# Kernel tuning notes

Measured on AMD Instinct MI355X. Metric: run time of the kernel, lower is better.

Reference implementation:

```python
import jax, jax.numpy as jnp
import numpy as np
import math

B, L, M, D, EL, H = 128, 105, 55, 256, 3, 1
PATCH = [3, 5, 7]

def pos_embed(T, d):
    pos = jnp.arange(T, dtype=jnp.float32)[:, None]
    div = jnp.exp(jnp.arange(0, d, 2, dtype=jnp.float32) * (-math.log(10000.0) / d))
    pe = jnp.zeros((T, d), dtype=jnp.float32)
    pe = pe.at[:, 0::2].set(jnp.sin(pos * div))
    pe = pe.at[:, 1::2].set(jnp.cos(pos * div))
    return pe

def circular_conv(x, w):
    # x: [N, T, Cin], w: [Dout, Cin, 3]; Conv1d kernel 3, circular padding 1, no bias
    xc = jnp.pad(x.transpose(0, 2, 1), ((0, 0), (0, 0), (1, 1)), mode='wrap')
    y = jax.lax.conv_general_dilated(xc, w, (1,), 'VALID', dimension_numbers=('NCH', 'OIH', 'NCH'))
    return y.transpose(0, 2, 1)

def _forward(x, conv_p0, conv_n0, conv_p1, conv_n1, conv_p2, conv_n2, Wq, bq, Wk, bk):
    convs = [(conv_p0, conv_n0), (conv_p1, conv_n1), (conv_p2, conv_n2)]
    # RevIN 'norm': per-sample standardization over time; stats are detached in torch
    mean = jax.lax.stop_gradient(jnp.mean(x, axis=1, keepdims=True))
    std = jax.lax.stop_gradient(jnp.sqrt(jnp.var(x, axis=1, keepdims=True) + 1e-5))
    xr = (x - mean) / std                      # [B, L, M]
    xt = xr.transpose(0, 2, 1)                 # [B, M, L]
    dk = D // H
    scale = 1.0 / math.sqrt(dk)
    series_list, prior_list = [], []
    for i, p in enumerate(PATCH):
        n = L // p
        # patch-size branch: (b m) n p -> embed over n with in_channels=p
        x_size = circular_conv(xt.reshape(B * M, n, p), convs[i][0]) + pos_embed(n, D)
        # patch-num branch: (b m) p n -> embed over p with in_channels=n
        x_num = circular_conv(xt.reshape(B * M, p, n), convs[i][1]) + pos_embed(p, D)
        for l in range(EL):
            def attn_mean(z):
                T = z.shape[1]
                q = (z @ Wq[l] + bq[l]).reshape(B * M, T, H, dk)
                k = (z @ Wk[l] + bk[l]).reshape(B * M, T, H, dk)
                a = jax.nn.softmax(scale * jnp.einsum('blhe,bshe->bhls', q, k), axis=-1)
                # fuse: mean over channel BEFORE expanding to window size
                # (repeat/tile commutes with the channel-mean, avoids [B*M,H,L,L])
                return a.reshape(B, M, H, T, T).mean(axis=1)   # [B, H, T, T]
            a_size = attn_mean(x_size)                          # [B, H, n, n]
            # einops repeat '(m rm) (n rn)': element-wise contiguous repeat
            series_list.append(jnp.repeat(jnp.repeat(a_size, p, axis=-2), p, axis=-1))
            a_num = attn_mean(x_num)                            # [B, H, p, p]
            # torch .repeat: tiling
            prior_list.append(jnp.tile(a_num, (1, 1, n, n)))
    # order: patch-major, layer-minor (matches the flattened lists)
    return jnp.stack(series_list), jnp.stack(prior_list)        # each [9, B, H, L, L]

def setup_inputs():
    key = jax.random.key(0)
    ks = jax.random.split(key, 12)
    s = 0.05
    inp = {"x": jax.random.normal(ks[0], (B, L, M), jnp.float32)}
    for i, p in enumerate(PATCH):
        inp[f"conv_p{i}"] = s * jax.random.normal(ks[1 + 2 * i], (D, p, 3), jnp.float32)
        inp[f"conv_n{i}"] = s * jax.random.normal(ks[2 + 2 * i], (D, L // p, 3), jnp.float32)
    inp["Wq"] = s * jax.random.normal(ks[7], (EL, D, D), jnp.float32)
    inp["bq"] = jnp.zeros((EL, D), jnp.float32)
    inp["Wk"] = s * jax.random.normal(ks[8], (EL, D, D), jnp.float32)
    inp["bk"] = jnp.zeros((EL, D), jnp.float32)
    return inp

def reference(x, conv_p0, conv_n0, conv_p1, conv_n1, conv_p2, conv_n2, Wq, bq, Wk, bk):
    return _forward(x, conv_p0, conv_n0, conv_p1, conv_n1, conv_p2, conv_n2, Wq, bq, Wk, bk)
```

## Files before the change

kernel.cpp:

```cpp
#include <hip/hip_runtime.h>
#include <hip/hip_bf16.h>

#define B_ 128
#define L_ 105
#define M_ 55
#define D_ 256
#define NCOMBO 18

#define WS_XT    0
#define WS_PE    739200
#define WS_LEFT  761216
#define WS_RIGHT 1258880
#define WS_MM    1756544
#define WS_MP    761216
#define WS_ACC   1258880
#define LR_STRIDE 27648
#define MM_STRIDE 11664
#define MP_STRIDE 12544
#define ACC_TOT  758016

#define WS_LRP        1966592
#define LRP_KZ_STRIDE 27648
#define LRP_C_STRIDE  110592
#define LRP_HALF      1990656
#define WS_NEED_BYTES ((size_t)(WS_LRP + 2 * LRP_HALF) * 4)

__constant__ int c_peOff[6] = {0, 35, 38, 59, 64, 79};
__constant__ int c_accbase[18] = {0,1225,2450, 3675,3684,3693, 3702,4143,4584,
                                  5025,5050,5075, 5100,5325,5550, 5775,5824,5873};

__device__ __forceinline__ void combo_dims(int c, int& i, int& br, int& l,
                                           int& p, int& n, int& Cin, int& T, int& J) {
    i = c / 6; br = (c % 6) / 3; l = c % 3;
    p = 3 + 2 * i;
    n = L_ / p;
    Cin = br ? n : p;
    T   = br ? p : n;
    J = 3 * Cin;
}

#define PREP_REVIN_BLOCKS 3520
#define PREP_BLOCKS (PREP_REVIN_BLOCKS + 6)
__global__ __launch_bounds__(256) void prep_kernel(const float* __restrict__ x,
                                                   float* __restrict__ ws) {
    int bid = blockIdx.x;
    if (bid < PREP_REVIN_BLOCKS) {
        int tid2 = threadIdx.x & 127;
        int half = threadIdx.x >> 7;
        int bm = bid * 2 + half;
        int b = bm / M_, m = bm % M_;
        __shared__ float s1[2][128], s2[2][128];
        float v = 0.f;
        if (tid2 < L_) v = x[(b * L_ + tid2) * M_ + m];
        s1[half][tid2] = v; s2[half][tid2] = v * v;
        __syncthreads();
        for (int off = 64; off > 0; off >>= 1) {
            if (tid2 < off) {
                s1[half][tid2] += s1[half][tid2 + off];
                s2[half][tid2] += s2[half][tid2 + off];
            }
            __syncthreads();
        }
        float mean = s1[half][0] * (1.f / L_);
        float var  = s2[half][0] * (1.f / L_) - mean * mean;
        float rstd = rsqrtf(var + 1e-5f);
        if (tid2 < L_) ws[WS_XT + bm * L_ + tid2] = (v - mean) * rstd;
    } else {
        int bi = bid - PREP_REVIN_BLOCKS;
        int i = bi / 2, br = bi % 2;
        int p = 3 + 2 * i, n = L_ / p;
        int T = br ? p : n;
        int d = threadIdx.x;
        float divv = expf(-(float)(d & ~1) * (logf(10000.f) / (float)D_));
        float* base = ws + WS_PE + c_peOff[bi] * D_;
        for (int t = 0; t < T; ++t) {
            float arg = (float)t * divv;
            base[t * D_ + d] = (d & 1) ? cosf(arg) : sinf(arg);
        }
    }
}

__global__ __launch_bounds__(256) void lr2_kernel(
                          const float* __restrict__ w0, const float* __restrict__ w1,
                          const float* __restrict__ w2c, const float* __restrict__ w3,
                          const float* __restrict__ w4, const float* __restrict__ w5,
                          const float* __restrict__ Wq, const float* __restrict__ bq,
                          const float* __restrict__ Wk, const float* __restrict__ bk,
                          float* __restrict__ ws) {
    int c = blockIdx.x;
    int i, br, l, p, n, Cin, T, J; combo_dims(c, i, br, l, p, n, Cin, T, J);
    int Mdim = J + T;
    int r0 = blockIdx.y * 8;
    if (r0 >= Mdim) return;
    int kz = blockIdx.z;
    int d0 = kz * 64;
    int wi = i * 2 + br;
    const float* conv = (wi == 0) ? w0 : (wi == 1) ? w1 : (wi == 2) ? w2c
                       : (wi == 3) ? w3 : (wi == 4) ? w4 : w5;
    __shared__ float S[8][64];
    int tid = threadIdx.x;
    for (int idx = tid; idx < 8 * 64; idx += 256) {
        int rr = idx >> 6, dd = idx & 63;
        int row = r0 + rr; float val = 0.f;
        int d = d0 + dd;
        if (row < J) val = conv[d * J + row];
        else if (row < Mdim) val = ws[WS_PE + (c_peOff[wi] + (row - J)) * D_ + d];
        S[rr][dd] = val;
    }
    __syncthreads();
    const float* wqp = Wq + l * D_ * D_;
    const float* wkp = Wk + l * D_ * D_;
    float accL[8], accR[8];
#pragma unroll
    for (int rr = 0; rr < 8; ++rr) { accL[rr] = 0.f; accR[rr] = 0.f; }
    int o = tid;
#pragma unroll 8
    for (int dd = 0; dd < 64; ++dd) {
        int d = d0 + dd;
        float wqv = wqp[d * D_ + o];
        float wkv = wkp[d * D_ + o];
#pragma unroll
        for (int rr = 0; rr < 8; ++rr) {
            float sv = S[rr][dd];
            accL[rr] += sv * wqv;
            accR[rr] += sv * wkv;
        }
    }
    float bqv = (kz == 0) ? bq[l * D_ + o] : 0.f;
    float bkv = (kz == 0) ? bk[l * D_ + o] : 0.f;
    float* Lp = ws + WS_LRP + c * LRP_C_STRIDE + kz * LRP_KZ_STRIDE;
    float* Rp = Lp + LRP_HALF;
#pragma unroll
    for (int rr = 0; rr < 8; ++rr) {
        int row = r0 + rr;
        if (row < Mdim) {
            float aq = (row >= J) ? bqv : 0.f;
            float ak = (row >= J) ? bkv : 0.f;
            Lp[row * D_ + o] = accL[rr] + aq;
            Rp[row * D_ + o] = accR[rr] + ak;
        }
    }
}

__global__ __launch_bounds__(256) void lr_kernel(
                          const float* __restrict__ w0, const float* __restrict__ w1,
                          const float* __restrict__ w2c, const float* __restrict__ w3,
                          const float* __restrict__ w4, const float* __restrict__ w5,
                          const float* __restrict__ Wq, const float* __restrict__ bq,
                          const float* __restrict__ Wk, const float* __restrict__ bk,
                          float* __restrict__ ws) {
    int c = blockIdx.x;
    int i, br, l, p, n, Cin, T, J; combo_dims(c, i, br, l, p, n, Cin, T, J);
    int Mdim = J + T;
    int r0 = blockIdx.y * 4;
    if (r0 >= Mdim) return;
    int wi = i * 2 + br;
    const float* conv = (wi == 0) ? w0 : (wi == 1) ? w1 : (wi == 2) ? w2c
                       : (wi == 3) ? w3 : (wi == 4) ? w4 : w5;
    __shared__ float S[4][256];
    int tid = threadIdx.x;
    for (int idx = tid; idx < 4 * 256; idx += 256) {
        int rr = idx >> 8, dd = idx & 255;
        int row = r0 + rr; float val = 0.f;
        if (row < J) val = conv[dd * J + row];
        else if (row < Mdim) val = ws[WS_PE + (c_peOff[wi] + (row - J)) * D_ + dd];
        S[rr][dd] = val;
    }
    __syncthreads();
    const float* wqp = Wq + l * D_ * D_;
    const float* wkp = Wk + l * D_ * D_;
    float accL[4], accR[4];
#pragma unroll
    for (int rr = 0; rr < 4; ++rr) { accL[rr] = 0.f; accR[rr] = 0.f; }
    int o = tid;
#pragma unroll 8
    for (int d = 0; d < D_; ++d) {
        float wqv = wqp[d * D_ + o];
        float wkv = wkp[d * D_ + o];
#pragma unroll
        for (int rr = 0; rr < 4; ++rr) {
            float sv = S[rr][d];
            accL[rr] += sv * wqv;
            accR[rr] += sv * wkv;
        }
    }
    float bqv = bq[l * D_ + o], bkv = bk[l * D_ + o];
#pragma unroll
    for (int rr = 0; rr < 4; ++rr) {
        int row = r0 + rr;
        if (row < Mdim) {
            float aq = (row >= J) ? bqv : 0.f;
            float ak = (row >= J) ? bkv : 0.f;
            ws[WS_LEFT  + c * LR_STRIDE + row * D_ + o] = accL[rr] + aq;
            ws[WS_RIGHT + c * LR_STRIDE + row * D_ + o] = accR[rr] + ak;
        }
    }
}

__global__ void mm_kernel(float* __restrict__ ws, int use_partial) {
    int c = blockIdx.x;
    int i, br, l, p, n, Cin, T, J; combo_dims(c, i, br, l, p, n, Cin, T, J);
    int Mdim = J + T;
    int tr = blockIdx.y / 7, tc = blockIdx.y % 7;
    int r0 = tr * 16, c0 = tc * 16;
    if (r0 >= Mdim || c0 >= Mdim) return;
    __shared__ __align__(16) float Lb[16][260], Rb[16][260];
    int tid = threadIdx.x;
    if (use_partial) {
        const float* Lp = ws + WS_LRP + c * LRP_C_STRIDE;
        const float* Rp = Lp + LRP_HALF;
        for (int idx = tid; idx < 16 * 256; idx += 256) {
            int rr = idx >> 8, d = idx & 255;
            int rL = r0 + rr, rR = c0 + rr;
            float lv = 0.f, rv = 0.f;
            if (rL < Mdim) {
                int base = rL * D_ + d;
                lv = Lp[base] + Lp[base + LRP_KZ_STRIDE]
                   + Lp[base + 2 * LRP_KZ_STRIDE] + Lp[base + 3 * LRP_KZ_STRIDE];
            }
            if (rR < Mdim) {
                int base = rR * D_ + d;
                rv = Rp[base] + Rp[base + LRP_KZ_STRIDE]
                   + Rp[base + 2 * LRP_KZ_STRIDE] + Rp[base + 3 * LRP_KZ_STRIDE];
            }
            Lb[rr][d] = lv; Rb[rr][d] = rv;
        }
    } else {
        for (int idx = tid; idx < 16 * 256; idx += 256) {
            int rr = idx >> 8, d = idx & 255;
            int rL = r0 + rr, rR = c0 + rr;
            Lb[rr][d] = (rL < Mdim) ? ws[WS_LEFT  + c * LR_STRIDE + rL * D_ + d] : 0.f;
            Rb[rr][d] = (rR < Mdim) ? ws[WS_RIGHT + c * LR_STRIDE + rR * D_ + d] : 0.f;
        }
    }
    __syncthreads();
    int rr = tid / 16, cc = tid % 16;
    const float4* lrow = (const float4*)(&Lb[rr][0]);
    const float4* rrow = (const float4*)(&Rb[cc][0]);
    float acc = 0.f;
#pragma unroll 8
    for (int d4 = 0; d4 < 64; ++d4) {
        float4 a = lrow[d4], bb = rrow[d4];
        acc += a.x * bb.x + a.y * bb.y + a.z * bb.z + a.w * bb.w;
    }
    int r = r0 + rr, cth = c0 + cc;
    if (r < Mdim && cth < Mdim)
        ws[WS_MM + c * MM_STRIDE + r * Mdim + cth] = acc;
}

__global__ void pack_kernel(float* __restrict__ ws) {
    int c = blockIdx.x;
    int i, br, l, p, n, Cin, T, J; combo_dims(c, i, br, l, p, n, Cin, T, J);
    int Mdim = J + T;
    int Cinp = (Cin + 3) & ~3;
    int Jp = 3 * Cinp;
    int T4 = (T + 3) & ~3;
    int W = Jp + T4;
    const float* MMc = ws + WS_MM + c * MM_STRIDE;
    float* Mp = ws + WS_MP + c * MP_STRIDE;
    for (int e = blockIdx.y * 256 + threadIdx.x; e < W * W; e += 16 * 256) {
        int r = e / W, o = e % W;
        int srcr = -1, srcc = -1;
        bool brow = false;
        if (r < Jp) {
            int k = r / Cinp, cin = r % Cinp;
            if (cin < Cin) srcr = cin * 3 + k;
        } else {
            int t = r - Jp;
            if (t < T) { srcr = J + t; brow = true; }
        }
        if (o < Jp) {
            int k2 = o / Cinp, cin2 = o % Cinp;
            if (cin2 < Cin) srcc = cin2 * 3 + k2;
        } else {
            int s = o - Jp;
            if (s < T) srcc = J + s;
        }
        float val;
        if (srcr >= 0 && srcc >= 0) val = MMc[srcr * Mdim + srcc];
        else if (brow && o >= Jp && srcc < 0) val = -1e30f;
        else val = 0.f;
        Mp[e] = val;
    }
}

__global__ void zero_acc(float* __restrict__ ws) {
    int idx = blockIdx.x * 256 + threadIdx.x;
    if (idx < ACC_TOT / 4) {
        float4 z; z.x = 0.f; z.y = 0.f; z.z = 0.f; z.w = 0.f;
        ((float4*)(ws + WS_ACC))[idx] = z;
    }
}

template<int P, int BR>
__global__ __launch_bounds__(256) void attn2(const float* __restrict__ ws,
                                             float* __restrict__ wsw) {
    constexpr int N    = L_ / P;
    constexpr int Cin  = BR ? N : P;
    constexpr int T    = BR ? P : N;
    constexpr int Cinp = (Cin + 3) & ~3;
    constexpr int Jp   = 3 * Cinp;
    constexpr int JP4  = Jp / 4;
    constexpr int T4   = (T + 3) & ~3;
    constexpr int W    = Jp + T4;
    constexpr int W4   = W / 4;
    constexpr int ST   = T4 + 1;
    constexpr int II   = (P - 3) / 2;
    constexpr int MC   = BR ? (P == 3 ? 12 : 8) : (P == 7 ? 8 : 4);
    constexpr int TH   = (BR == 0 && P == 3) ? 2 : 1;
    constexpr int TSUB = (T + TH - 1) / TH;
    constexpr int GR   = MC * TSUB + 1;
    constexpr int NT   = (MC / 4) * TSUB * W4;
    constexpr int TPB  = (NT + 255) / 256;
    constexpr int MCQ  = MC / 4;
    constexpr int CQ   = Cinp / 4;
    constexpr int CQP  = CQ | 1;
    constexpr int S4N  = T4 / 4;
    constexpr int XTR4 = Cinp * MCQ + 1;

    constexpr int OFF_X2A = 0;
    constexpr int SZ_X2A  = MC * T * CQP * 4;
    constexpr int OFF_G   = OFF_X2A + SZ_X2A;
    constexpr int SZ_G    = 4 * W4 * GR;
    constexpr int OFF_X2T = OFF_G + SZ_G;
    constexpr int SZ_X2T  = T * XTR4 * 4;
    constexpr int OFF_MSL = OFF_X2T + SZ_X2T;
    constexpr int SZ_MSL  = BR ? 0 : Cinp * W;
    constexpr int OFF_S   = OFF_X2T;
    constexpr int SZ_S    = MC * TSUB * ST;
    constexpr int END_A   = OFF_MSL + SZ_MSL;
    constexpr int END_B   = OFF_S + SZ_S;
    constexpr int TOT     = (END_A > END_B) ? END_A : END_B;
    static_assert(TOT * 4 <= 65536, "LDS budget");

    __shared__ __align__(16) float smem[TOT];
    const int tid = threadIdx.x;
    const int b = blockIdx.x, l = blockIdx.y;
    const int sp = blockIdx.z / TH;
    const int th = blockIdx.z % TH;
    const int t0 = th * TSUB;
    const int TC = (T - t0 < TSUB) ? (T - t0) : TSUB;
    const int c = II * 6 + BR * 3 + l;
    const int m0 = sp * MC;
    const int vm = (M_ - m0 < MC) ? (M_ - m0) : MC;

    const float*  Mpg  = ws + WS_MP + c * MP_STRIDE;
    const float4* Mpg4 = (const float4*)Mpg;

    for (int e = tid; e < MC * T * CQP * 4; e += 256) {
        int cin  = e % (CQP * 4);
        int trow = (e / (CQP * 4)) % T;
        int mcol = e / (CQP * 4 * T);
        float v = 0.f;
        if (cin < Cin && m0 + mcol < M_)
            v = ws[WS_XT + (size_t)(b * M_ + m0 + mcol) * L_ + trow * Cin + cin];
        smem[OFF_X2A + e] = v;
    }
    for (int e = tid; e < T * XTR4 * 4; e += 256) {
        int w    = e % (XTR4 * 4);
        int trow = e / (XTR4 * 4);
        float v = 0.f;
        if (w < Cinp * MC) {
            int mcol = w % MC, cin = w / MC;
            if (cin < Cin && m0 + mcol < M_)
                v = ws[WS_XT + (size_t)(b * M_ + m0 + mcol) * L_ + trow * Cin + cin];
        }
        smem[OFF_X2T + e] = v;
    }
    __syncthreads();

    const float4* X2T4 = (const float4*)(smem + OFF_X2T);
    const float4* X2A4 = (const float4*)(smem + OFF_X2A);
    float4*       MSL4 = (float4*)(smem + OFF_MSL);
    float4*       G4w  = (float4*)(smem + OFF_G);
    const float4* G4   = (const float4*)(smem + OFF_G);

    float a[TPB][4][4];
#pragma unroll
    for (int tt = 0; tt < TPB; ++tt) {
        int q = tid + tt * 256;
        if (q < NT) {
            int o4 = q % W4, tl = (q / W4) % TSUB;
            if (tl < TC) {
                float4 bv = Mpg4[(Jp + t0 + tl) * W4 + o4];
#pragma unroll
                for (int am = 0; am < 4; ++am) {
                    a[tt][am][0] = bv.x; a[tt][am][1] = bv.y;
                    a[tt][am][2] = bv.z; a[tt][am][3] = bv.w;
                }
            }
        }
    }
    if constexpr (BR == 0) {
        for (int k = 0; k < 3; ++k) {
            for (int e = tid; e < Cinp * W4; e += 256)
                MSL4[e] = Mpg4[k * Cinp * W4 + e];
            __syncthreads();
#pragma unroll
            for (int tt = 0; tt < TPB; ++tt) {
                int q = tid + tt * 256;
                if (q < NT) {
                    int o4 = q % W4, tl = (q / W4) % TSUB, m4 = q / (W4 * TSUB);
                    if (tl < TC) {
                        int trow = t0 + tl + k - 1;
                        if (trow < 0) trow += T;
                        if (trow >= T) trow -= T;
                        const float4* xp = X2T4 + trow * XTR4 + m4;
                        const float4* mp = MSL4 + o4;
#pragma unroll 4
                        for (int cin = 0; cin < Cinp; ++cin) {
                            float4 x4 = xp[cin * MCQ];
                            float4 mv = mp[cin * W4];
#pragma unroll
                            for (int aq = 0; aq < 4; ++aq) {
                                float m = (aq == 0) ? mv.x : (aq == 1) ? mv.y
                                        : (aq == 2) ? mv.z : mv.w;
                                a[tt][0][aq] += x4.x * m;
                                a[tt][1][aq] += x4.y * m;
                                a[tt][2][aq] += x4.z * m;
                                a[tt][3][aq] += x4.w * m;
                            }
                        }
                    }
                }
            }
            __syncthreads();
        }
    } else {
        __syncthreads();
#pragma unroll
        for (int k = 0; k < 3; ++k) {
#pragma unroll
            for (int tt = 0; tt < TPB; ++tt) {
                int q = tid + tt * 256;
                if (q < NT) {
                    int o4 = q % W4, tl = (q / W4) % TSUB, m4 = q / (W4 * TSUB);
                    if (tl < TC) {
                        int trow = t0 + tl + k - 1;
                        if (trow < 0) trow += T;
                        if (trow >= T) trow -= T;
                        const float4* xp = X2T4 + trow * XTR4 + m4;
                        const float4* mp = Mpg4 + k * Cinp * W4 + o4;
#pragma unroll 4
                        for (int cin = 0; cin < Cinp; ++cin) {
                            float4 x4 = xp[cin * MCQ];
                            float4 mv = mp[cin * W4];
#pragma unroll
                            for (int aq = 0; aq < 4; ++aq) {
                                float m = (aq == 0) ? mv.x : (aq == 1) ? mv.y
                                        : (aq == 2) ? mv.z : mv.w;
                                a[tt][0][aq] += x4.x * m;
                                a[tt][1][aq] += x4.y * m;
                                a[tt][2][aq] += x4.z * m;
                                a[tt][3][aq] += x4.w * m;
                            }
                        }
                    }
                }
            }
        }
    }
#pragma unroll
    for (int tt = 0; tt < TPB; ++tt) {
        int q = tid + tt * 256;
        if (q < NT) {
            int o4 = q % W4, tl = (q / W4) % TSUB, m4 = q / (W4 * TSUB);
            if (tl < TC) {
#pragma unroll
                for (int am = 0; am < 4; ++am) {
                    float4 o;
                    o.x = a[tt][am][0]; o.y = a[tt][am][1];
                    o.z = a[tt][am][2]; o.w = a[tt][am][3];
                    G4w[o4 * GR + (m4 * 4 + am) * TSUB + tl] = o;
                }
            }
        }
    }
    __syncthreads();

    for (int it = tid; it < MC * TSUB * S4N; it += 256) {
        int tl = it % TSUB;
        int s4 = (it / TSUB) % S4N;
        int mc = it / (TSUB * S4N);
        if (tl >= TC) continue;
        int mrow = mc * TSUB + tl;
        float4 bi = G4[(JP4 + s4) * GR + mrow];
        float acc[4] = {bi.x, bi.y, bi.z, bi.w};
#pragma unroll 2
        for (int cinq = 0; cinq < CQ; ++cinq) {
            float4 xr[6];
#pragma unroll
            for (int kk = 0; kk < 6; ++kk) {
                int r = s4 * 4 - 1 + kk;
                if (r < 0) r += T;
                if (r >= T) r -= T;
                xr[kk] = X2A4[(mc * T + r) * CQP + cinq];
            }
#pragma unroll
            for (int k = 0; k < 3; ++k) {
                float4 g = G4[(k * CQ + cinq) * GR + mrow];
#pragma unroll
                for (int q = 0; q < 4; ++q) {
                    float4 x4 = xr[q + k];
                    acc[q] += g.x * x4.x + g.y * x4.y + g.z * x4.z + g.w * x4.w;
                }
            }
        }
#pragma unroll
        for (int q = 0; q < 4; ++q)
            smem[OFF_S + (mc * TSUB + tl) * ST + s4 * 4 + q] = 0.0625f * acc[q];
    }
    __syncthreads();

    for (int rid = tid; rid < MC * TSUB; rid += 256) {
        int mc = rid / TSUB, tl = rid % TSUB;
        if (tl >= TC) continue;
        int base = OFF_S + (mc * TSUB + tl) * ST;
        float pr[T4];
#pragma unroll
        for (int s = 0; s < T4; ++s) pr[s] = smem[base + s];
        float mx = -1e30f;
#pragma unroll
        for (int s = 0; s < T4; ++s) mx = fmaxf(mx, pr[s]);
        float sum = 0.f;
#pragma unroll
        for (int s = 0; s < T4; ++s) { pr[s] = __expf(pr[s] - mx); sum += pr[s]; }
        float inv = 1.f / sum;
#pragma unroll
        for (int s = 0; s < T; ++s) smem[base + s] = pr[s] * inv;
    }
    __syncthreads();

    float* accp = wsw + WS_ACC + c_accbase[c] * 128 + b * T * T;
    for (int e = tid; e < TC * T; e += 256) {
        int tl = e / T, s = e % T;
        float v = 0.f;
        for (int mc = 0; mc < vm; ++mc)
            v += smem[OFF_S + (mc * TSUB + tl) * ST + s];
        atomicAdd(&accp[(t0 + tl) * T + s], v);
    }
}

template<int P, int BR>
__device__ __forceinline__ void expand_body(const float* __restrict__ acc,
                                            float* __restrict__ outp) {
    constexpr int T = BR ? P : (L_ / P);
    for (int idx = threadIdx.x; idx < L_ * L_; idx += 256) {
        int r = idx / L_, c2 = idx % L_;
        int rt = BR ? (r % P) : (r / P);
        int ct = BR ? (c2 % P) : (c2 / P);
        outp[idx] = acc[rt * T + ct];
    }
}

__global__ __launch_bounds__(256) void expand_kernel(const float* __restrict__ ws,
                                                     float* __restrict__ out) {
    int c = blockIdx.x, b = blockIdx.y;
    int i = c / 6, br = (c % 6) / 3, l = c % 3;
    int p = 3 + 2 * i;
    int T = br ? p : (L_ / p);
    __shared__ float sAcc[1232];
    int abase = c_accbase[c] * 128 + b * T * T;
    for (int idx = threadIdx.x; idx < T * T; idx += 256)
        sAcc[idx] = ws[WS_ACC + abase + idx] * (1.f / (float)M_);
    __syncthreads();
    float* outp = out + ((size_t)(br * 9 + i * 3 + l) * B_ + (size_t)b) * (size_t)(L_ * L_);
    int key = i * 2 + br;
    switch (key) {
        case 0: expand_body<3, 0>(sAcc, outp); break;
        case 1: expand_body<3, 1>(sAcc, outp); break;
        case 2: expand_body<5, 0>(sAcc, outp); break;
        case 3: expand_body<5, 1>(sAcc, outp); break;
        case 4: expand_body<7, 0>(sAcc, outp); break;
        case 5: expand_body<7, 1>(sAcc, outp); break;
    }
}

extern "C" void kernel_launch(void* const* d_in, const int* in_sizes, int n_in,
                              void* d_out, int out_size, void* d_ws, size_t ws_size,
                              hipStream_t stream) {
    const float* x   = (const float*)d_in[0];
    const float* cp0 = (const float*)d_in[1];
    const float* cn0 = (const float*)d_in[2];
    const float* cp1 = (const float*)d_in[3];
    const float* cn1 = (const float*)d_in[4];
    const float* cp2 = (const float*)d_in[5];
    const float* cn2 = (const float*)d_in[6];
    const float* Wq  = (const float*)d_in[7];
    const float* bq  = (const float*)d_in[8];
    const float* Wk  = (const float*)d_in[9];
    const float* bk  = (const float*)d_in[10];
    float* ws = (float*)d_ws;
    float* out = (float*)d_out;

    const int use_partial = (ws_size >= WS_NEED_BYTES) ? 1 : 0;

    hipLaunchKernelGGL(prep_kernel, dim3(PREP_BLOCKS), dim3(256), 0, stream, x, ws);
    if (use_partial) {
        hipLaunchKernelGGL(lr2_kernel, dim3(NCOMBO, 14, 4), dim3(256), 0, stream,
                           cp0, cn0, cp1, cn1, cp2, cn2, Wq, bq, Wk, bk, ws);
    } else {
        hipLaunchKernelGGL(lr_kernel, dim3(NCOMBO, 27), dim3(256), 0, stream,
                           cp0, cn0, cp1, cn1, cp2, cn2, Wq, bq, Wk, bk, ws);
    }
    hipLaunchKernelGGL(mm_kernel, dim3(NCOMBO, 49), dim3(256), 0, stream, ws, use_partial);
    hipLaunchKernelGGL(pack_kernel, dim3(NCOMBO, 16), dim3(256), 0, stream, ws);
    hipLaunchKernelGGL(zero_acc, dim3((ACC_TOT / 4 + 255) / 256), dim3(256), 0, stream, ws);

    hipLaunchKernelGGL((attn2<3, 0>), dim3(B_, 3, 28), dim3(256), 0, stream, ws, ws);
    hipLaunchKernelGGL((attn2<3, 1>), dim3(B_, 3, 5),  dim3(256), 0, stream, ws, ws);
    hipLaunchKernelGGL((attn2<5, 0>), dim3(B_, 3, 14), dim3(256), 0, stream, ws, ws);
    hipLaunchKernelGGL((attn2<5, 1>), dim3(B_, 3, 7),  dim3(256), 0, stream, ws, ws);
    hipLaunchKernelGGL((attn2<7, 0>), dim3(B_, 3, 7),  dim3(256), 0, stream, ws, ws);
    hipLaunchKernelGGL((attn2<7, 1>), dim3(B_, 3, 7),  dim3(256), 0, stream, ws, ws);

    hipLaunchKernelGGL(expand_kernel, dim3(NCOMBO, B_), dim3(256), 0, stream, ws, out);
}
```

Baseline: 444.5 us.

## Fuse pack into mm_kernel writes and load full Mp slice into LDS once

The mm_kernel now writes its results directly in the packed, padded Mp layout, and the padding entries are initialised in prep_kernel. This removes the separate pack_kernel launch when the partial workspace path is active. The BR==0 attention kernel now loads all three k-slices of Mp into LDS once instead of reloading per k with barriers in between. The cost is more LDS per block, which may reduce occupancy.

```diff
diff --git a/kernel.cpp b/kernel.cpp
--- a/kernel.cpp
+++ b/kernel.cpp
@@ -40,7 +40,7 @@
 }
 
 #define PREP_REVIN_BLOCKS 3520
-#define PREP_BLOCKS (PREP_REVIN_BLOCKS + 6)
+#define PREP_BLOCKS (PREP_REVIN_BLOCKS + 6 + NCOMBO)
 __global__ __launch_bounds__(256) void prep_kernel(const float* __restrict__ x,
                                                    float* __restrict__ ws) {
     int bid = blockIdx.x;
@@ -65,7 +65,7 @@
         float var  = s2[half][0] * (1.f / L_) - mean * mean;
         float rstd = rsqrtf(var + 1e-5f);
         if (tid2 < L_) ws[WS_XT + bm * L_ + tid2] = (v - mean) * rstd;
-    } else {
+    } else if (bid < PREP_REVIN_BLOCKS + 6) {
         int bi = bid - PREP_REVIN_BLOCKS;
         int i = bi / 2, br = bi % 2;
         int p = 3 + 2 * i, n = L_ / p;
@@ -76,6 +76,22 @@
         for (int t = 0; t < T; ++t) {
             float arg = (float)t * divv;
             base[t * D_ + d] = (d & 1) ? cosf(arg) : sinf(arg);
+        }
+    } else {
+        int c = bid - (PREP_REVIN_BLOCKS + 6);
+        int i, br, l, p, n, Cin, T, J; combo_dims(c, i, br, l, p, n, Cin, T, J);
+        int Cinp = (Cin + 3) & ~3;
+        int Jp = 3 * Cinp;
+        int T4 = (T + 3) & ~3;
+        int W = Jp + T4;
+        float* Mp = ws + WS_MP + c * MP_STRIDE;
+        for (int e = threadIdx.x; e < W * W; e += 256) {
+            int r = e / W, o = e % W;
+            bool vr   = (r < Jp) ? ((r % Cinp) < Cin) : (r - Jp < T);
+            bool brow = (r >= Jp) && (r - Jp < T);
+            bool vc   = (o < Jp) ? ((o % Cinp) < Cin) : (o - Jp < T);
+            if (!(vr && vc))
+                Mp[e] = (brow && o >= Jp && !vc) ? -1e30f : 0.f;
         }
     }
 }
@@ -244,8 +260,18 @@
         acc += a.x * bb.x + a.y * bb.y + a.z * bb.z + a.w * bb.w;
     }
     int r = r0 + rr, cth = c0 + cc;
-    if (r < Mdim && cth < Mdim)
-        ws[WS_MM + c * MM_STRIDE + r * Mdim + cth] = acc;
+    if (r < Mdim && cth < Mdim) {
+        if (use_partial) {
+            int Cinp = (Cin + 3) & ~3;
+            int Jp = 3 * Cinp;
+            int W = Jp + ((T + 3) & ~3);
+            int rp = (r   < J) ? ((r   % 3) * Cinp + r   / 3) : (Jp + r   - J);
+            int op = (cth < J) ? ((cth % 3) * Cinp + cth / 3) : (Jp + cth - J);
+            ws[WS_MP + c * MP_STRIDE + rp * W + op] = acc;
+        } else {
+            ws[WS_MM + c * MM_STRIDE + r * Mdim + cth] = acc;
+        }
+    }
 }
 
 __global__ void pack_kernel(float* __restrict__ ws) {
@@ -325,7 +351,7 @@
     constexpr int OFF_X2T = OFF_G + SZ_G;
     constexpr int SZ_X2T  = T * XTR4 * 4;
     constexpr int OFF_MSL = OFF_X2T + SZ_X2T;
-    constexpr int SZ_MSL  = BR ? 0 : Cinp * W;
+    constexpr int SZ_MSL  = BR ? 0 : Jp * W;
     constexpr int OFF_S   = OFF_X2T;
     constexpr int SZ_S    = MC * TSUB * ST;
     constexpr int END_A   = OFF_MSL + SZ_MSL;
@@ -367,11 +393,15 @@
         }
         smem[OFF_X2T + e] = v;
     }
+    float4* MSL4 = (float4*)(smem + OFF_MSL);
+    if constexpr (BR == 0) {
+        for (int e = tid; e < Jp * W4; e += 256)
+            MSL4[e] = ((const float4*)Mpg)[e];
+    }
     __syncthreads();
 
     const float4* X2T4 = (const float4*)(smem + OFF_X2T);
     const float4* X2A4 = (const float4*)(smem + OFF_X2A);
-    float4*       MSL4 = (float4*)(smem + OFF_MSL);
     float4*       G4w  = (float4*)(smem + OFF_G);
     const float4* G4   = (const float4*)(smem + OFF_G);
 
@@ -391,69 +421,34 @@
             }
         }
     }
-    if constexpr (BR == 0) {
-        for (int k = 0; k < 3; ++k) {
-            for (int e = tid; e < Cinp * W4; e += 256)
-                MSL4[e] = Mpg4[k * Cinp * W4 + e];
-            __syncthreads();
-#pragma unroll
-            for (int tt = 0; tt < TPB; ++tt) {
-                int q = tid + tt * 256;
-                if (q < NT) {
-                    int o4 = q % W4, tl = (q / W4) % TSUB, m4 = q / (W4 * TSUB);
-                    if (tl < TC) {
-                        int trow = t0 + tl + k - 1;
-                        if (trow < 0) trow += T;
-                        if (trow >= T) trow -= T;
-                        const float4* xp = X2T4 + trow * XTR4 + m4;
-                        const float4* mp = MSL4 + o4;
+#pragma unroll
+    for (int k = 0; k < 3; ++k) {
+#pragma unroll
+        for (int tt = 0; tt < TPB; ++tt) {
+            int q = tid + tt * 256;
+            if (q < NT) {
+                int o4 = q % W4, tl = (q / W4) % TSUB, m4 = q / (W4 * TSUB);
+                if (tl < TC) {
+                    int trow = t0 + tl + k - 1;
+                    if (trow < 0) trow += T;
+                    if (trow >= T) trow -= T;
+                    const float4* xp = X2T4 + trow * XTR4 + m4;
 #pragma unroll 4
-                        for (int cin = 0; cin < Cinp; ++cin) {
-                            float4 x4 = xp[cin * MCQ];
-                            float4 mv = mp[cin * W4];
-#pragma unroll
-                            for (int aq = 0; aq < 4; ++aq) {
-                                float m = (aq == 0) ? mv.x : (aq == 1) ? mv.y
-                                        : (aq == 2) ? mv.z : mv.w;
-                                a[tt][0][aq] += x4.x * m;
-                                a[tt][1][aq] += x4.y * m;
-                                a[tt][2][aq] += x4.z * m;
-                                a[tt][3][aq] += x4.w * m;
-                            }
-                        }
-                    }
-                }
-            }
-            __syncthreads();
-        }
-    } else {
-        __syncthreads();
-#pragma unroll
-        for (int k = 0; k < 3; ++k) {
-#pragma unroll
-            for (int tt = 0; tt < TPB; ++tt) {
-                int q = tid + tt * 256;
-                if (q < NT) {
-                    int o4 = q % W4, tl = (q / W4) % TSUB, m4 = q / (W4 * TSUB);
-                    if (tl < TC) {
-                        int trow = t0 + tl + k - 1;
-                        if (trow < 0) trow += T;
-                        if (trow >= T) trow -= T;
-                        const float4* xp = X2T4 + trow * XTR4 + m4;
-                        const float4* mp = Mpg4 + k * Cinp * W4 + o4;
-#pragma unroll 4
-                        for (int cin = 0; cin < Cinp; ++cin) {
-                            float4 x4 = xp[cin * MCQ];
-                            float4 mv = mp[cin * W4];
-#pragma unroll
-                            for (int aq = 0; aq < 4; ++aq) {
-                                float m = (aq == 0) ? mv.x : (aq == 1) ? mv.y
-                                        : (aq == 2) ? mv.z : mv.w;
-                                a[tt][0][aq] += x4.x * m;
-                                a[tt][1][aq] += x4.y * m;
-                                a[tt][2][aq] += x4.z * m;
-                                a[tt][3][aq] += x4.w * m;
-                            }
+                    for (int cin = 0; cin < Cinp; ++cin) {
+                        float4 x4 = xp[cin * MCQ];
+                        float4 mv;
+                        if constexpr (BR == 0)
+                            mv = MSL4[k * Cinp * W4 + cin * W4 + o4];
+                        else
+                            mv = Mpg4[k * Cinp * W4 + cin * W4 + o4];
+#pragma unroll
+                        for (int aq = 0; aq < 4; ++aq) {
+                            float m = (aq == 0) ? mv.x : (aq == 1) ? mv.y
+                                    : (aq == 2) ? mv.z : mv.w;
+                            a[tt][0][aq] += x4.x * m;
+                            a[tt][1][aq] += x4.y * m;
+                            a[tt][2][aq] += x4.z * m;
+                            a[tt][3][aq] += x4.w * m;
                         }
                     }
                 }
@@ -604,7 +599,9 @@
                            cp0, cn0, cp1, cn1, cp2, cn2, Wq, bq, Wk, bk, ws);
     }
     hipLaunchKernelGGL(mm_kernel, dim3(NCOMBO, 49), dim3(256), 0, stream, ws, use_partial);
-    hipLaunchKernelGGL(pack_kernel, dim3(NCOMBO, 16), dim3(256), 0, stream, ws);
+    if (!use_partial) {
+        hipLaunchKernelGGL(pack_kernel, dim3(NCOMBO, 16), dim3(256), 0, stream, ws);
+    }
     hipLaunchKernelGGL(zero_acc, dim3((ACC_TOT / 4 + 255) / 256), dim3(256), 0, stream, ws);
 
     hipLaunchKernelGGL((attn2<3, 0>), dim3(B_, 3, 28), dim3(256), 0, stream, ws, ws);
```

After: 439.6 us. No clear change (-1.1%).
